# Optimization experiments

Measured on AMD Instinct MI355X. Metric: run time of the kernel, lower is better.

Reference implementation:

```python
import jax, jax.numpy as jnp
import numpy as np

NUM_GRAPHS = 128


def _gcn_conv(x, W, b, src, dst, norm, n_nodes):
    # PyG GCNConv: linear transform, then symmetric-normalized scatter-add aggregation
    h = x @ W                                  # [N, out]
    msg = norm[:, None] * h[src]               # [E+N, out] gathered messages
    out = jax.ops.segment_sum(msg, dst, num_segments=n_nodes)
    return out + b


def setup_inputs() -> dict:
    key = jax.random.key(0)
    ks = jax.random.split(key, 12)
    N, E, H, GE, C = 100000, 1000000, 64, 64, 5
    x = jax.random.normal(ks[0], (N, 2), dtype=jnp.float32)
    edge_index = jax.random.randint(ks[1], (2, E), 0, N, dtype=jnp.int32)
    batch = jnp.sort(jax.random.randint(ks[2], (N,), 0, NUM_GRAPHS, dtype=jnp.int32))
    graph_embedding = jax.random.normal(ks[3], (NUM_GRAPHS, GE), dtype=jnp.float32)
    s = lambda k, shape, fan: jax.random.normal(k, shape, dtype=jnp.float32) * (1.0 / np.sqrt(fan))
    W1 = s(ks[4], (2, H), 2); b1 = jnp.zeros((H,), jnp.float32)
    W2 = s(ks[5], (H, H), H); b2 = jnp.zeros((H,), jnp.float32)
    W3 = s(ks[6], (H, H), H); b3 = jnp.zeros((H,), jnp.float32)
    Wl = s(ks[7], (H + GE, C), H + GE); bl = jnp.zeros((C,), jnp.float32)
    return {"x": x, "edge_index": edge_index, "batch": batch,
            "graph_embedding": graph_embedding,
            "W1": W1, "b1": b1, "W2": W2, "b2": b2, "W3": W3, "b3": b3,
            "Wl": Wl, "bl": bl}


def reference(x, edge_index, batch, graph_embedding, W1, b1, W2, b2, W3, b3, Wl, bl):
    N = x.shape[0]
    loops = jnp.arange(N, dtype=edge_index.dtype)
    src = jnp.concatenate([edge_index[0], loops])   # add self-loops
    dst = jnp.concatenate([edge_index[1], loops])
    deg = jax.ops.segment_sum(jnp.ones_like(dst, dtype=x.dtype), dst, num_segments=N)
    dinv = jnp.where(deg > 0, jax.lax.rsqrt(deg), 0.0)
    norm = dinv[src] * dinv[dst]                    # [E+N]

    h = jax.nn.relu(_gcn_conv(x, W1, b1, src, dst, norm, N))
    h = jax.nn.relu(_gcn_conv(h, W2, b2, src, dst, norm, N))
    h = _gcn_conv(h, W3, b3, src, dst, norm, N)

    # global mean pool over graphs
    sums = jax.ops.segment_sum(h, batch, num_segments=NUM_GRAPHS)
    cnts = jax.ops.segment_sum(jnp.ones((N,), x.dtype), batch, num_segments=NUM_GRAPHS)
    pooled = sums / jnp.maximum(cnts, 1.0)[:, None]

    z = jnp.concatenate([pooled, graph_embedding], axis=1) @ Wl + bl
    return jax.nn.log_softmax(z, axis=1)
```

## Files before the change

kernel.cpp:

```cpp
#include <hip/hip_runtime.h>
#include <hip/hip_bf16.h>
#include <math.h>

#define NG 128
#define CHUNKB 2048
#define NBIN 512
#define EWIN 256
#define STAGE_CAP 6144

typedef __attribute__((ext_vector_type(8))) short short8;
typedef __attribute__((ext_vector_type(4))) float float4v;
typedef __attribute__((ext_vector_type(4))) uint uint4v;

__global__ void k_bin_hist(const int* __restrict__ dst, int* __restrict__ hist,
                           int e, int nb, float* __restrict__ sums,
                           const float* __restrict__ W2, const float* __restrict__ W3,
                           __hip_bfloat16* __restrict__ Wf2, __hip_bfloat16* __restrict__ Wf3) {
    __shared__ int h[NBIN];
    int blk = blockIdx.x;
    if (blk >= nb) {
        int ex = blk - nb;
        if (ex == 0) {
            for (int i = threadIdx.x; i < NG * 64; i += 256) sums[i] = 0.0f;
        } else {
            const float* W = (ex == 2) ? W3 : W2;
            __hip_bfloat16* Wf = (ex == 2) ? Wf3 : Wf2;
            for (int t = threadIdx.x; t < 512; t += 256) {
                int c = t >> 6, l = t & 63;
                int jt = c >> 1, half = c & 1, nn = l & 15, q = l >> 4;
                #pragma unroll
                for (int j = 0; j < 8; j++) {
                    int k = half * 32 + q * 8 + j;
                    Wf[t * 8 + j] = __float2bfloat16(W[k * 64 + jt * 16 + nn]);
                }
            }
        }
        return;
    }
    for (int i = threadIdx.x; i < NBIN; i += 256) h[i] = 0;
    __syncthreads();
    int base = blk * CHUNKB;
    int lim = e - base; if (lim > CHUNKB) lim = CHUNKB;
    for (int k = threadIdx.x; k < lim; k += 256)
        atomicAdd(&h[dst[base + k] >> 8], 1);
    __syncthreads();
    for (int b = threadIdx.x; b < NBIN; b += 256) hist[b * nb + blk] = h[b];
}

__global__ void __launch_bounds__(512) genscan1(int* __restrict__ a, int* __restrict__ bsums, int n) {
    __shared__ int s[512];
    int tid = threadIdx.x;
    int i = blockIdx.x * 512 + tid;
    int v = (i < n) ? a[i] : 0;
    s[tid] = v;
    __syncthreads();
    for (int d = 1; d < 512; d <<= 1) {
        int t = (tid >= d) ? s[tid - d] : 0;
        __syncthreads();
        s[tid] += t;
        __syncthreads();
    }
    if (i < n) a[i] = s[tid] - v;
    if (tid == 511) bsums[blockIdx.x] = s[511];
}

__global__ void __launch_bounds__(512) genscan2(int* __restrict__ bsums, int nb) {
    __shared__ int s[512];
    int tid = threadIdx.x;
    int v = (tid < nb) ? bsums[tid] : 0;
    s[tid] = v;
    __syncthreads();
    for (int d = 1; d < 512; d <<= 1) {
        int t = (tid >= d) ? s[tid - d] : 0;
        __syncthreads();
        s[tid] += t;
        __syncthreads();
    }
    if (tid < nb) bsums[tid] = s[tid] - v;
}

__global__ void k_bin_scatter(const int* __restrict__ srcs, const int* __restrict__ dsts,
                              const int* __restrict__ offsets, const int* __restrict__ bsums,
                              int* __restrict__ outbuf, int e, int nb) {
    __shared__ int hcnt[NBIN];
    __shared__ int lstart[NBIN];
    __shared__ int ss[256];
    __shared__ int stage[CHUNKB];
    __shared__ int sbuck[CHUNKB];
    int tid = threadIdx.x, blk = blockIdx.x, base = blk * CHUNKB;
    int lim = e - base; if (lim > CHUNKB) lim = CHUNKB;
    for (int i = tid; i < NBIN; i += 256) hcnt[i] = 0;
    __syncthreads();
    for (int k = tid; k < lim; k += 256)
        atomicAdd(&hcnt[dsts[base + k] >> 8], 1);
    __syncthreads();
    int c0 = hcnt[2 * tid], c1 = hcnt[2 * tid + 1];
    int sum = c0 + c1;
    ss[tid] = sum;
    __syncthreads();
    for (int d = 1; d < 256; d <<= 1) {
        int t = (tid >= d) ? ss[tid - d] : 0;
        __syncthreads();
        ss[tid] += t;
        __syncthreads();
    }
    int excl = ss[tid] - sum;
    lstart[2 * tid] = excl;
    lstart[2 * tid + 1] = excl + c0;
    __syncthreads();
    hcnt[2 * tid] = excl;
    hcnt[2 * tid + 1] = excl + c0;
    __syncthreads();
    for (int k = tid; k < lim; k += 256) {
        int s = srcs[base + k], d = dsts[base + k];
        int bk = d >> 8;
        int p = atomicAdd(&hcnt[bk], 1);
        stage[p] = ((d & 255) << 24) | s;
        sbuck[p] = bk;
    }
    __syncthreads();
    for (int i = tid; i < NBIN; i += 256) {
        int gi = i * nb + blk;
        lstart[i] = offsets[gi] + bsums[gi >> 9] - lstart[i];
    }
    __syncthreads();
    for (int p = tid; p < lim; p += 256)
        outbuf[lstart[sbuck[p]] + p] = stage[p];
}

__global__ void k_csrAB(const int* __restrict__ ebuck, const int* __restrict__ offsets,
                        const int* __restrict__ bsums, const float* __restrict__ x,
                        int* __restrict__ row_ptr, float* __restrict__ dinv,
                        float2* __restrict__ xs, int* __restrict__ csr,
                        int n, int nb, int e_total) {
    __shared__ int lcnt[256];
    __shared__ int ssc[256];
    __shared__ int rstart[256];
    __shared__ int stage[STAGE_CAP];
    int b = blockIdx.x, tid = threadIdx.x, n0 = b << 8;
    lcnt[tid] = 0;
    __syncthreads();
    int i0 = b * nb, i1 = (b + 1) * nb;
    int e0 = offsets[i0] + bsums[i0 >> 9];
    int e1 = offsets[i1] + bsums[i1 >> 9];
    int cnt = e1 - e0;
    bool fast = (cnt <= STAGE_CAP);
    if (fast) {
        for (int i = e0 + tid; i < e1; i += 256) {
            int p = ebuck[i];
            stage[i - e0] = p;
            atomicAdd(&lcnt[(uint)p >> 24], 1);
        }
    } else {
        for (int i = e0 + tid; i < e1; i += 256)
            atomicAdd(&lcnt[(uint)ebuck[i] >> 24], 1);
    }
    __syncthreads();
    int v = lcnt[tid];
    ssc[tid] = v;
    __syncthreads();
    for (int d = 1; d < 256; d <<= 1) {
        int t = (tid >= d) ? ssc[tid - d] : 0;
        __syncthreads();
        ssc[tid] += t;
        __syncthreads();
    }
    int rs = e0 + ssc[tid] - v;
    rstart[tid] = rs;
    int node = n0 + tid;
    if (node < n) {
        row_ptr[node] = rs;
        float dv = rsqrtf((float)v + 1.0f);
        dinv[node] = dv;
        const float2* x2 = (const float2*)x;
        float2 xi = x2[node];
        xs[node] = make_float2(xi.x * dv, xi.y * dv);
        if (node == n - 1) row_ptr[n] = e_total;
    }
    lcnt[tid] = 0;
    __syncthreads();
    if (fast) {
        for (int i = tid; i < cnt; i += 256) {
            int p = stage[i];
            int li = (uint)p >> 24;
            int r = atomicAdd(&lcnt[li], 1);
            csr[rstart[li] + r] = p & 0xFFFFFF;
        }
    } else {
        for (int i = e0 + tid; i < e1; i += 256) {
            int p = ebuck[i];
            int li = (uint)p >> 24;
            int r = atomicAdd(&lcnt[li], 1);
            csr[rstart[li] + r] = p & 0xFFFFFF;
        }
    }
}

__global__ void k_layer1(const int* __restrict__ row_ptr, const int* __restrict__ edges,
                         const float2* __restrict__ xs, const float* __restrict__ dinv,
                         const float* __restrict__ W1, const float* __restrict__ b1,
                         __hip_bfloat16* __restrict__ h, int n) {
    __shared__ float w1s[128];
    __shared__ float b1s[64];
    if (threadIdx.x < 128) w1s[threadIdx.x] = W1[threadIdx.x];
    if (threadIdx.x < 64) b1s[threadIdx.x] = b1[threadIdx.x];
    __syncthreads();
    int i = blockIdx.x * blockDim.x + threadIdx.x;
    if (i >= n) return;
    float dd = dinv[i];
    float2 xi = xs[i];
    float a0 = xi.x, a1 = xi.y;
    int lo = row_ptr[i], hi = row_ptr[i + 1];
    int k = lo;
    for (; k + 4 <= hi; k += 4) {
        int s0 = edges[k], s1 = edges[k + 1], s2 = edges[k + 2], s3 = edges[k + 3];
        float2 v0 = xs[s0], v1 = xs[s1], v2 = xs[s2], v3 = xs[s3];
        a0 += v0.x + v1.x + v2.x + v3.x;
        a1 += v0.y + v1.y + v2.y + v3.y;
    }
    for (; k < hi; k++) {
        float2 v = xs[edges[k]];
        a0 += v.x;
        a1 += v.y;
    }
    a0 *= dd; a1 *= dd;
    short8* hv = reinterpret_cast<short8*>(h + (size_t)i * 64);
    #pragma unroll
    for (int g = 0; g < 8; g++) {
        short8 pack;
        #pragma unroll
        for (int j = 0; j < 8; j++) {
            int col = g * 8 + j;
            float v = fmaxf(a0 * w1s[col] + a1 * w1s[64 + col] + b1s[col], 0.0f);
            v *= dd;
            __hip_bfloat16 bv = __float2bfloat16(v);
            pack[j] = *reinterpret_cast<short*>(&bv);
        }
        hv[g] = pack;
    }
}

static __device__ __forceinline__ void acc8(float* a, uint4v v) {
    #pragma unroll
    for (int i = 0; i < 4; i++) {
        uint u = v[i];
        a[2 * i]     += __int_as_float(u << 16);
        a[2 * i + 1] += __int_as_float(u & 0xffff0000u);
    }
}

template <bool FAST>
static __device__ __forceinline__ void agg_group(int lo, int cnt, int mc, int c,
        const int* __restrict__ gE, const int* EW, int wave_lo,
        const uint4v* __restrict__ hin4, float* acc) {
    for (int j = 0; j < mc; j += 2) {
        bool ok0 = j < cnt, ok1 = j + 1 < cnt;
        int e0 = ok0 ? lo + j : wave_lo;
        int e1 = ok1 ? lo + j + 1 : wave_lo;
        int s0 = FAST ? EW[e0 - wave_lo] : gE[e0];
        int s1 = FAST ? EW[e1 - wave_lo] : gE[e1];
        uint4v v0 = hin4[(size_t)s0 * 8 + c];
        uint4v v1 = hin4[(size_t)s1 * 8 + c];
        if (!ok0) v0 = (uint4v){0u, 0u, 0u, 0u};
        if (!ok1) v1 = (uint4v){0u, 0u, 0u, 0u};
        acc8(acc, v0);
        acc8(acc, v1);
    }
}

template <int RELU, int POOL>
__global__ void __launch_bounds__(64, 8) k_aggLin(const int* __restrict__ row_ptr,
                                                  const int* __restrict__ edges,
                                                  const __hip_bfloat16* __restrict__ hin,
                                                  const float* __restrict__ dinv,
                                                  const __hip_bfloat16* __restrict__ Wf,
                                                  const float* __restrict__ b,
                                                  __hip_bfloat16* __restrict__ hout,
                                                  const int* __restrict__ batch,
                                                  float* __restrict__ sums, int n) {
    __shared__ __attribute__((aligned(16))) __hip_bfloat16 T[16 * 72];
    __shared__ int EW[EWIN];
    int lane = threadIdx.x;
    int nb0 = blockIdx.x * 16;
    if (nb0 >= n) return;
    int g = lane >> 3;
    int c = lane & 7;
    const uint4v* hin4 = reinterpret_cast<const uint4v*>(hin);

    int bidx = nb0 + (lane < 16 ? lane : 16);
    if (bidx > n) bidx = n;
    int rp = row_ptr[bidx];
    int wave_lo = __shfl(rp, 0);
    int wave_hi = __shfl(rp, 16);
    int cnt_all = wave_hi - wave_lo;
    bool fast = (cnt_all <= EWIN);
    if (fast)
        for (int i = lane; i < cnt_all; i += 64) EW[i] = edges[wave_lo + i];

    #pragma unroll
    for (int h8 = 0; h8 < 2; h8++) {
        int nn = h8 * 8 + g;
        int node = nb0 + nn;
        float acc[8] = {0.f, 0.f, 0.f, 0.f, 0.f, 0.f, 0.f, 0.f};
        int lo = __shfl(rp, nn);
        int hi = __shfl(rp, nn + 1);
        int cnt = (node < n) ? (hi - lo) : 0;
        int mc = cnt;
        mc = max(mc, __shfl_xor(mc, 8));
        mc = max(mc, __shfl_xor(mc, 16));
        mc = max(mc, __shfl_xor(mc, 32));
        if (node < n)
            acc8(acc, hin4[(size_t)node * 8 + c]);
        if (fast) agg_group<true >(lo, cnt, mc, c, edges, EW, wave_lo, hin4, acc);
        else      agg_group<false>(lo, cnt, mc, c, edges, EW, wave_lo, hin4, acc);
        float dv = (node < n) ? dinv[node] : 0.0f;
        uint4v pk;
        #pragma unroll
        for (int i = 0; i < 4; i++) {
            __hip_bfloat16 bx = __float2bfloat16(acc[2 * i] * dv);
            __hip_bfloat16 by = __float2bfloat16(acc[2 * i + 1] * dv);
            pk[i] = (uint)(*reinterpret_cast<unsigned short*>(&bx)) |
                    ((uint)(*reinterpret_cast<unsigned short*>(&by)) << 16);
        }
        *reinterpret_cast<uint4v*>(&T[nn * 72 + c * 8]) = pk;
    }

    int m = lane & 15, q = lane >> 4;
    short8 a0 = *reinterpret_cast<const short8*>(&T[m * 72 + q * 8]);
    short8 a1 = *reinterpret_cast<const short8*>(&T[m * 72 + 32 + q * 8]);
    int lastn = nb0 + 15 < n ? nb0 + 15 : n - 1;
    bool onegraph = POOL && (nb0 + 15 < n) && (batch[nb0] == batch[lastn]);
    int gA = POOL ? batch[nb0] : 0;
    float dvs[4];
    if (!POOL) {
        #pragma unroll
        for (int r = 0; r < 4; r++) {
            int node = nb0 + q * 4 + r;
            dvs[r] = node < n ? dinv[node] : 0.0f;
        }
    }
    #pragma unroll
    for (int jt = 0; jt < 4; jt++) {
        short8 bf0 = *reinterpret_cast<const short8*>(Wf + ((size_t)(jt * 2 + 0) * 64 + lane) * 8);
        short8 bf1 = *reinterpret_cast<const short8*>(Wf + ((size_t)(jt * 2 + 1) * 64 + lane) * 8);
        float4v d = {0.0f, 0.0f, 0.0f, 0.0f};
        d = __builtin_amdgcn_mfma_f32_16x16x32_bf16(a0, bf0, d, 0, 0, 0);
        d = __builtin_amdgcn_mfma_f32_16x16x32_bf16(a1, bf1, d, 0, 0, 0);
        float bias = b[jt * 16 + m];
        if (POOL) {
            if (onegraph) {
                float s = (d[0] + bias) + (d[1] + bias) + (d[2] + bias) + (d[3] + bias);
                s += __shfl_xor(s, 16);
                s += __shfl_xor(s, 32);
                if (q == 0) atomicAdd(&sums[gA * 64 + jt * 16 + m], s);
            } else {
                #pragma unroll
                for (int r = 0; r < 4; r++) {
                    int node = nb0 + q * 4 + r;
                    if (node < n)
                        atomicAdd(&sums[batch[node] * 64 + jt * 16 + m], d[r] + bias);
                }
            }
        } else {
            #pragma unroll
            for (int r = 0; r < 4; r++) {
                int node = nb0 + q * 4 + r;
                if (node < n) {
                    float v = d[r] + bias;
                    if (RELU) v = fmaxf(v, 0.0f);
                    v *= dvs[r];
                    hout[(size_t)node * 64 + jt * 16 + m] = __float2bfloat16(v);
                }
            }
        }
    }
}

__device__ inline int lower_bound_i(const int* __restrict__ a, int n, int key) {
    int lo = 0, hi = n;
    while (lo < hi) {
        int mid = (lo + hi) >> 1;
        if (a[mid] < key) lo = mid + 1; else hi = mid;
    }
    return lo;
}

__global__ void k_head(const float* __restrict__ sums, const int* __restrict__ batch,
                       const float* __restrict__ ge, const float* __restrict__ Wl,
                       const float* __restrict__ bl, float* __restrict__ out,
                       int n, int ng) {
    int g = blockIdx.x * blockDim.x + threadIdx.x;
    if (g < ng) {
        int lo = lower_bound_i(batch, n, g);
        int hi = lower_bound_i(batch, n, g + 1);
        float c = fmaxf((float)(hi - lo), 1.0f);
        float z[5];
        for (int cl = 0; cl < 5; cl++) z[cl] = bl[cl];
        for (int k = 0; k < 64; k++) {
            float p = sums[g * 64 + k] / c;
            for (int cl = 0; cl < 5; cl++) z[cl] += p * Wl[k * 5 + cl];
        }
        for (int k = 0; k < 64; k++) {
            float p = ge[g * 64 + k];
            for (int cl = 0; cl < 5; cl++) z[cl] += p * Wl[(64 + k) * 5 + cl];
        }
        float m = z[0];
        for (int cl = 1; cl < 5; cl++) m = fmaxf(m, z[cl]);
        float s = 0.0f;
        for (int cl = 0; cl < 5; cl++) s += expf(z[cl] - m);
        float lse = m + logf(s);
        for (int cl = 0; cl < 5; cl++) out[g * 5 + cl] = z[cl] - lse;
    }
}

#define ALIGN16(x) (((x) + 15) & ~(size_t)15)

extern "C" void kernel_launch(void* const* d_in, const int* in_sizes, int n_in,
                              void* d_out, int out_size, void* d_ws, size_t ws_size,
                              hipStream_t stream) {
    const float* x    = (const float*)d_in[0];
    const int*   ei   = (const int*)d_in[1];
    const int*   batch= (const int*)d_in[2];
    const float* ge   = (const float*)d_in[3];
    const float* W1   = (const float*)d_in[4];
    const float* b1   = (const float*)d_in[5];
    const float* W2   = (const float*)d_in[6];
    const float* b2   = (const float*)d_in[7];
    const float* W3   = (const float*)d_in[8];
    const float* b3   = (const float*)d_in[9];
    const float* Wl   = (const float*)d_in[10];
    const float* bl   = (const float*)d_in[11];
    float* out = (float*)d_out;

    const int N = in_sizes[0] / 2;
    const int E = in_sizes[1] / 2;
    const int* src = ei;
    const int* dst = ei + E;
    const int NBUK = (N + 255) >> 8;
    const int nbC  = (E + CHUNKB - 1) / CHUNKB;

    char* wsb = (char*)d_ws;
    float* dinv   = (float*)wsb;                wsb += ALIGN16((size_t)N * 4);
    float2* xs    = (float2*)wsb;               wsb += ALIGN16((size_t)N * 8);
    __hip_bfloat16* h16 = (__hip_bfloat16*)wsb;  wsb += ALIGN16((size_t)64 * N * 2);
    __hip_bfloat16* buf2= (__hip_bfloat16*)wsb;  wsb += ALIGN16((size_t)64 * N * 2);
    float* sums   = (float*)wsb;                wsb += ALIGN16((size_t)NG * 64 * 4);
    __hip_bfloat16* Wf2 = (__hip_bfloat16*)wsb; wsb += ALIGN16((size_t)4096 * 2);
    __hip_bfloat16* Wf3 = (__hip_bfloat16*)wsb; wsb += ALIGN16((size_t)4096 * 2);
    int*   ebuck  = (int*)wsb;                  wsb += ALIGN16((size_t)E * 4);
    int*   csr    = (int*)wsb;                  wsb += ALIGN16((size_t)E * 4);
    int*   row_ptr= (int*)wsb;                  wsb += ALIGN16((size_t)(N + 1) * 4);
    int*   hist   = (int*)wsb;                  wsb += ALIGN16((size_t)NBIN * nbC * 4);
    int*   bsums  = (int*)wsb;                  wsb += 512 * 4;

    const int BS = 256;
    int gN   = (N + BS - 1) / BS;
    int gF   = (N + 15) / 16;
    int nH   = NBIN * nbC;
    int gH   = (nH + 511) / 512;

    k_bin_hist<<<nbC + 3, BS, 0, stream>>>(dst, hist, E, nbC, sums, W2, W3, Wf2, Wf3);
    genscan1<<<gH, 512, 0, stream>>>(hist, bsums, nH);
    genscan2<<<1, 512, 0, stream>>>(bsums, gH);
    k_bin_scatter<<<nbC, BS, 0, stream>>>(src, dst, hist, bsums, ebuck, E, nbC);
    k_csrAB<<<NBUK, BS, 0, stream>>>(ebuck, hist, bsums, x, row_ptr, dinv, xs, csr,
                                     N, nbC, E);

    k_layer1<<<gN, BS, 0, stream>>>(row_ptr, csr, xs, dinv, W1, b1, h16, N);

    k_aggLin<1, 0><<<gF, 64, 0, stream>>>(row_ptr, csr, h16, dinv, Wf2, b2, buf2,
                                          nullptr, nullptr, N);

    k_aggLin<0, 1><<<gF, 64, 0, stream>>>(row_ptr, csr, buf2, dinv, Wf3, b3, nullptr,
                                          batch, sums, N);

    k_head<<<1, 128, 0, stream>>>(sums, batch, ge, Wl, bl, out, N, NG);
}
```

Measured before the change: 195.4 us.

## Replace per-chunk histogram scan with global bin counts and atomic cursors

The per-chunk x per-bin histogram and its two-kernel global prefix scan are replaced by a 512-entry global bin count, accumulated with atomics. Each scatter block rescans those counts locally and claims its slot inside each bin with an atomicAdd on a per-bin cursor. This removes two kernel launches and the large histogram buffer traffic, and the sums zeroing moves into a memset. In exchange, the order of edges within a bucket becomes nondeterministic, and every block redoes a small 512-entry scan.

```diff
diff --git a/kernel.cpp b/kernel.cpp
--- a/kernel.cpp
+++ b/kernel.cpp
@@ -12,27 +12,23 @@
 typedef __attribute__((ext_vector_type(4))) float float4v;
 typedef __attribute__((ext_vector_type(4))) uint uint4v;
 
-__global__ void k_bin_hist(const int* __restrict__ dst, int* __restrict__ hist,
-                           int e, int nb, float* __restrict__ sums,
+__global__ void k_bin_hist(const int* __restrict__ dst, int* __restrict__ gcnt,
+                           int e, int nb,
                            const float* __restrict__ W2, const float* __restrict__ W3,
                            __hip_bfloat16* __restrict__ Wf2, __hip_bfloat16* __restrict__ Wf3) {
     __shared__ int h[NBIN];
     int blk = blockIdx.x;
     if (blk >= nb) {
         int ex = blk - nb;
-        if (ex == 0) {
-            for (int i = threadIdx.x; i < NG * 64; i += 256) sums[i] = 0.0f;
-        } else {
-            const float* W = (ex == 2) ? W3 : W2;
-            __hip_bfloat16* Wf = (ex == 2) ? Wf3 : Wf2;
-            for (int t = threadIdx.x; t < 512; t += 256) {
-                int c = t >> 6, l = t & 63;
-                int jt = c >> 1, half = c & 1, nn = l & 15, q = l >> 4;
-                #pragma unroll
-                for (int j = 0; j < 8; j++) {
-                    int k = half * 32 + q * 8 + j;
-                    Wf[t * 8 + j] = __float2bfloat16(W[k * 64 + jt * 16 + nn]);
-                }
+        const float* W = ex ? W3 : W2;
+        __hip_bfloat16* Wf = ex ? Wf3 : Wf2;
+        for (int t = threadIdx.x; t < 512; t += 256) {
+            int c = t >> 6, l = t & 63;
+            int jt = c >> 1, half = c & 1, nn = l & 15, q = l >> 4;
+            #pragma unroll
+            for (int j = 0; j < 8; j++) {
+                int k = half * 32 + q * 8 + j;
+                Wf[t * 8 + j] = __float2bfloat16(W[k * 64 + jt * 16 + nn]);
             }
         }
         return;
@@ -44,43 +40,14 @@
     for (int k = threadIdx.x; k < lim; k += 256)
         atomicAdd(&h[dst[base + k] >> 8], 1);
     __syncthreads();
-    for (int b = threadIdx.x; b < NBIN; b += 256) hist[b * nb + blk] = h[b];
-}
-
-__global__ void __launch_bounds__(512) genscan1(int* __restrict__ a, int* __restrict__ bsums, int n) {
-    __shared__ int s[512];
-    int tid = threadIdx.x;
-    int i = blockIdx.x * 512 + tid;
-    int v = (i < n) ? a[i] : 0;
-    s[tid] = v;
-    __syncthreads();
-    for (int d = 1; d < 512; d <<= 1) {
-        int t = (tid >= d) ? s[tid - d] : 0;
-        __syncthreads();
-        s[tid] += t;
-        __syncthreads();
-    }
-    if (i < n) a[i] = s[tid] - v;
-    if (tid == 511) bsums[blockIdx.x] = s[511];
-}
-
-__global__ void __launch_bounds__(512) genscan2(int* __restrict__ bsums, int nb) {
-    __shared__ int s[512];
-    int tid = threadIdx.x;
-    int v = (tid < nb) ? bsums[tid] : 0;
-    s[tid] = v;
-    __syncthreads();
-    for (int d = 1; d < 512; d <<= 1) {
-        int t = (tid >= d) ? s[tid - d] : 0;
-        __syncthreads();
-        s[tid] += t;
-        __syncthreads();
-    }
-    if (tid < nb) bsums[tid] = s[tid] - v;
+    for (int b = threadIdx.x; b < NBIN; b += 256) {
+        int v = h[b];
+        if (v) atomicAdd(&gcnt[b], v);
+    }
 }
 
 __global__ void k_bin_scatter(const int* __restrict__ srcs, const int* __restrict__ dsts,
-                              const int* __restrict__ offsets, const int* __restrict__ bsums,
+                              const int* __restrict__ gcnt, int* __restrict__ gcur,
                               int* __restrict__ outbuf, int e, int nb) {
     __shared__ int hcnt[NBIN];
     __shared__ int lstart[NBIN];
@@ -119,30 +86,58 @@
         sbuck[p] = bk;
     }
     __syncthreads();
-    for (int i = tid; i < NBIN; i += 256) {
-        int gi = i * nb + blk;
-        lstart[i] = offsets[gi] + bsums[gi >> 9] - lstart[i];
+    int g0 = gcnt[2 * tid], g1 = gcnt[2 * tid + 1];
+    int gs = g0 + g1;
+    ss[tid] = gs;
+    __syncthreads();
+    for (int d = 1; d < 256; d <<= 1) {
+        int t = (tid >= d) ? ss[tid - d] : 0;
+        __syncthreads();
+        ss[tid] += t;
+        __syncthreads();
+    }
+    int gexcl = ss[tid] - gs;
+    if (c0 > 0) {
+        int r = atomicAdd(&gcur[2 * tid], c0);
+        lstart[2 * tid] = gexcl + r - lstart[2 * tid];
+    }
+    if (c1 > 0) {
+        int r = atomicAdd(&gcur[2 * tid + 1], c1);
+        lstart[2 * tid + 1] = (gexcl + g0) + r - lstart[2 * tid + 1];
     }
     __syncthreads();
     for (int p = tid; p < lim; p += 256)
         outbuf[lstart[sbuck[p]] + p] = stage[p];
 }
 
-__global__ void k_csrAB(const int* __restrict__ ebuck, const int* __restrict__ offsets,
-                        const int* __restrict__ bsums, const float* __restrict__ x,
+__global__ void k_csrAB(const int* __restrict__ ebuck, const int* __restrict__ gcnt,
+                        const float* __restrict__ x,
                         int* __restrict__ row_ptr, float* __restrict__ dinv,
                         float2* __restrict__ xs, int* __restrict__ csr,
-                        int n, int nb, int e_total) {
+                        int n, int e_total) {
     __shared__ int lcnt[256];
     __shared__ int ssc[256];
     __shared__ int rstart[256];
+    __shared__ int exc[NBIN];
     __shared__ int stage[STAGE_CAP];
     int b = blockIdx.x, tid = threadIdx.x, n0 = b << 8;
     lcnt[tid] = 0;
-    __syncthreads();
-    int i0 = b * nb, i1 = (b + 1) * nb;
-    int e0 = offsets[i0] + bsums[i0 >> 9];
-    int e1 = offsets[i1] + bsums[i1 >> 9];
+    int g0 = gcnt[2 * tid], g1 = gcnt[2 * tid + 1];
+    int gs = g0 + g1;
+    ssc[tid] = gs;
+    __syncthreads();
+    for (int d = 1; d < 256; d <<= 1) {
+        int t = (tid >= d) ? ssc[tid - d] : 0;
+        __syncthreads();
+        ssc[tid] += t;
+        __syncthreads();
+    }
+    int gexcl = ssc[tid] - gs;
+    exc[2 * tid] = gexcl;
+    exc[2 * tid + 1] = gexcl + g0;
+    __syncthreads();
+    int e0 = exc[b];
+    int e1 = e0 + gcnt[b];
     int cnt = e1 - e0;
     bool fast = (cnt <= STAGE_CAP);
     if (fast) {
@@ -445,26 +440,22 @@
     __hip_bfloat16* h16 = (__hip_bfloat16*)wsb;  wsb += ALIGN16((size_t)64 * N * 2);
     __hip_bfloat16* buf2= (__hip_bfloat16*)wsb;  wsb += ALIGN16((size_t)64 * N * 2);
     float* sums   = (float*)wsb;                wsb += ALIGN16((size_t)NG * 64 * 4);
+    int*   gcnt   = (int*)wsb;                  wsb += ALIGN16((size_t)NBIN * 4);
+    int*   gcur   = (int*)wsb;                  wsb += ALIGN16((size_t)NBIN * 4);
     __hip_bfloat16* Wf2 = (__hip_bfloat16*)wsb; wsb += ALIGN16((size_t)4096 * 2);
     __hip_bfloat16* Wf3 = (__hip_bfloat16*)wsb; wsb += ALIGN16((size_t)4096 * 2);
     int*   ebuck  = (int*)wsb;                  wsb += ALIGN16((size_t)E * 4);
     int*   csr    = (int*)wsb;                  wsb += ALIGN16((size_t)E * 4);
     int*   row_ptr= (int*)wsb;                  wsb += ALIGN16((size_t)(N + 1) * 4);
-    int*   hist   = (int*)wsb;                  wsb += ALIGN16((size_t)NBIN * nbC * 4);
-    int*   bsums  = (int*)wsb;                  wsb += 512 * 4;
 
     const int BS = 256;
     int gN   = (N + BS - 1) / BS;
     int gF   = (N + 15) / 16;
-    int nH   = NBIN * nbC;
-    int gH   = (nH + 511) / 512;
-
-    k_bin_hist<<<nbC + 3, BS, 0, stream>>>(dst, hist, E, nbC, sums, W2, W3, Wf2, Wf3);
-    genscan1<<<gH, 512, 0, stream>>>(hist, bsums, nH);
-    genscan2<<<1, 512, 0, stream>>>(bsums, gH);
-    k_bin_scatter<<<nbC, BS, 0, stream>>>(src, dst, hist, bsums, ebuck, E, nbC);
-    k_csrAB<<<NBUK, BS, 0, stream>>>(ebuck, hist, bsums, x, row_ptr, dinv, xs, csr,
-                                     N, nbC, E);
+
+    hipMemsetAsync(sums, 0, (size_t)NG * 64 * 4 + 2 * ALIGN16((size_t)NBIN * 4), stream);
+    k_bin_hist<<<nbC + 2, BS, 0, stream>>>(dst, gcnt, E, nbC, W2, W3, Wf2, Wf3);
+    k_bin_scatter<<<nbC, BS, 0, stream>>>(src, dst, gcnt, gcur, ebuck, E, nbC);
+    k_csrAB<<<NBUK, BS, 0, stream>>>(ebuck, gcnt, x, row_ptr, dinv, xs, csr, N, E);
 
     k_layer1<<<gN, BS, 0, stream>>>(row_ptr, csr, xs, dinv, W1, b1, h16, N);
 
```

Result: slower. 215.1 us (+10.1%).
